# Kernel optimization log

Hardware: AMD Instinct MI355X
Metric: run time of the kernel (lower is better)

The kernel has to match this reference:

```python
import jax, jax.numpy as jnp
import numpy as np

DIM = 2048
DIM_INNER = 4096
D_STATE = 64
D_CONV = 4
HEADDIM = 128
NHEADS = DIM_INNER // HEADDIM  # 32
CHUNK = 256
BATCH = 1
SEQ = 2048
CONV_DIM = DIM_INNER + 2 * D_STATE           # 4224
D_IN_PROJ = 2 * DIM_INNER + 2 * D_STATE + NHEADS  # 8352


def setup_inputs() -> dict:
    key = jax.random.key(0)
    ks = jax.random.split(key, 8)
    x = jax.random.normal(ks[0], (BATCH, SEQ, DIM), jnp.float32)
    in_proj_w = jax.random.normal(ks[1], (D_IN_PROJ, DIM), jnp.float32) * 0.02
    conv_w = jax.random.normal(ks[2], (CONV_DIM, D_CONV), jnp.float32) * 0.2
    conv_b = jnp.zeros((CONV_DIM,), jnp.float32)
    dt_bias = jax.random.normal(ks[3], (NHEADS,), jnp.float32) * 0.1
    A_log = jnp.log(jax.random.uniform(ks[4], (NHEADS,), jnp.float32, 1.0, 16.0))
    D = jnp.ones((NHEADS,), jnp.float32)
    norm_w = jnp.ones((DIM_INNER,), jnp.float32)
    out_proj_w = jax.random.normal(ks[5], (DIM, DIM_INNER), jnp.float32) * 0.02
    return dict(x=x, in_proj_w=in_proj_w, conv_w=conv_w, conv_b=conv_b,
                dt_bias=dt_bias, A_log=A_log, D=D, norm_w=norm_w,
                out_proj_w=out_proj_w)


def _segsum(a):
    # a: [..., T]; out[..., i, j] = sum_{k=j+1..i} a[..., k] for i>=j else -inf
    T = a.shape[-1]
    cs = jnp.cumsum(a, axis=-1)
    seg = cs[..., :, None] - cs[..., None, :]
    mask = jnp.tril(jnp.ones((T, T), bool))
    return jnp.where(mask, seg, -jnp.inf)


def _ssd(x, A, Bm, Cm, chunk):
    # x: [b,l,h,p], A: [b,l,h], Bm/Cm: [b,l,n] (ngroups=1, group dim squeezed)
    b, l, h, p = x.shape
    n = Bm.shape[-1]
    c = l // chunk
    x = x.reshape(b, c, chunk, h, p)
    A = A.reshape(b, c, chunk, h).transpose(0, 3, 1, 2)  # [b,h,c,l]
    Bm = Bm.reshape(b, c, chunk, n)
    Cm = Cm.reshape(b, c, chunk, n)
    A_cumsum = jnp.cumsum(A, axis=-1)                    # [b,h,c,l]
    Lmat = jnp.exp(_segsum(A))                           # [b,h,c,l,l]
    # intra-chunk (diagonal) contribution
    Y_diag = jnp.einsum('bcln,bcsn,bhcls,bcshp->bclhp', Cm, Bm, Lmat, x)
    # per-chunk states
    decay_states = jnp.exp(A_cumsum[..., -1:] - A_cumsum)
    states = jnp.einsum('bcln,bhcl,bclhp->bchpn', Bm, decay_states, x)
    states = jnp.concatenate([jnp.zeros_like(states[:, :1]), states], axis=1)
    # inter-chunk recurrence
    A_last = jnp.pad(A_cumsum[..., -1], ((0, 0), (0, 0), (1, 0)))  # [b,h,c+1]
    decay_chunk = jnp.exp(_segsum(A_last))
    new_states = jnp.einsum('bhzc,bchpn->bzhpn', decay_chunk, states)
    states, final_state = new_states[:, :-1], new_states[:, -1]
    # state -> output (off-diagonal) contribution
    state_decay_out = jnp.exp(A_cumsum)
    Y_off = jnp.einsum('bcln,bchpn,bhcl->bclhp', Cm, states, state_decay_out)
    return (Y_diag + Y_off).reshape(b, l, h, p), final_state


def reference(x, in_proj_w, conv_w, conv_b, dt_bias, A_log, D, norm_w, out_proj_w):
    B, L, _ = x.shape
    zxbcdt = x @ in_proj_w.T                              # [B,L,8352]
    z = zxbcdt[..., :DIM_INNER]
    xBC = zxbcdt[..., DIM_INNER:DIM_INNER + CONV_DIM]
    dt = jax.nn.softplus(zxbcdt[..., -NHEADS:] + dt_bias)  # [B,L,H]
    # causal depthwise conv1d over time (pad d_conv-1 on the left)
    xc = xBC.transpose(0, 2, 1)                           # [B,conv_dim,L]
    xc = jax.lax.conv_general_dilated(
        xc, conv_w[:, None, :], (1,), [(D_CONV - 1, 0)],
        dimension_numbers=('NCH', 'OIH', 'NCH'), feature_group_count=CONV_DIM)
    xc = xc + conv_b[None, :, None]
    xBC = jax.nn.silu(xc).transpose(0, 2, 1)              # [B,L,conv_dim]
    xs = xBC[..., :DIM_INNER].reshape(B, L, NHEADS, HEADDIM)
    Bmat = xBC[..., DIM_INNER:DIM_INNER + D_STATE]
    Cmat = xBC[..., DIM_INNER + D_STATE:]
    A = -jnp.exp(A_log)                                   # [H]
    y, final_state = _ssd(xs * dt[..., None], A * dt, Bmat, Cmat, CHUNK)
    y = y + xs * D[:, None]
    y = y.reshape(B, L, DIM_INNER)
    # gated RMSNorm: x * silu(z), then rms_norm with weight
    g = y * jax.nn.silu(z)
    g = g * jax.lax.rsqrt(jnp.mean(g * g, axis=-1, keepdims=True) + 1e-5) * norm_w
    return g @ out_proj_w.T
```

## Files before the change

kernel.cpp:

```cpp
#include <hip/hip_runtime.h>

typedef short v8s __attribute__((ext_vector_type(8)));
typedef float v4f __attribute__((ext_vector_type(4)));

#define L_SEQ  2048
#define DPROJ  8352
#define CONVD  4224
#define DIN    4096
#define NH     32
#define HD     128
#define NSTATE 64
#define NCHUNK 8
#define CKLEN  256

#define GLOAD_LDS16(gp, lp) \
  __builtin_amdgcn_global_load_lds((const __attribute__((address_space(1))) void*)(gp), \
                                   (__attribute__((address_space(3))) void*)(lp), 16, 0, 0)

__device__ __forceinline__ unsigned short to_bf16(float f) {
  unsigned u = __float_as_uint(f);
  return (unsigned short)((u + 0x7fffu + ((u >> 16) & 1u)) >> 16);
}

__global__ void cvt_bf16_kernel(const float* __restrict__ in,
                                unsigned short* __restrict__ out, int n) {
  int i = (blockIdx.x * 256 + threadIdx.x) * 8;
  if (i + 8 <= n) {
    float4 a = *(const float4*)(in + i);
    float4 b = *(const float4*)(in + i + 4);
    v8s r;
    r[0] = (short)to_bf16(a.x); r[1] = (short)to_bf16(a.y);
    r[2] = (short)to_bf16(a.z); r[3] = (short)to_bf16(a.w);
    r[4] = (short)to_bf16(b.x); r[5] = (short)to_bf16(b.y);
    r[6] = (short)to_bf16(b.z); r[7] = (short)to_bf16(b.w);
    *(v8s*)(out + i) = r;
  }
}


#define BAR    __builtin_amdgcn_s_barrier()
#define SCHEDB __builtin_amdgcn_sched_barrier(0)
#define LGKM0  asm volatile("s_waitcnt lgkmcnt(0)" ::: "memory")
#define VMCNT4 asm volatile("s_waitcnt vmcnt(4)" ::: "memory")

#define RDA(bu, mh) do { \
  _Pragma("unroll") \
  for (int i = 0; i < 4; ++i) \
    _Pragma("unroll") \
    for (int s = 0; s < 2; ++s) { \
      int row_ = (mh) * 128 + wm * 64 + i * 16 + lrow; \
      int off_ = row_ * 128 + s * 64 + lquad * 16; \
      off_ ^= ((off_ >> 7) & 7) << 4; \
      a8[i][s] = *(const v8s*)((const char*)smem + (bu) * 32768 + off_); \
    } \
} while (0)

#define RDB(bu, nh) do { \
  _Pragma("unroll") \
  for (int j = 0; j < 2; ++j) \
    _Pragma("unroll") \
    for (int s = 0; s < 2; ++s) { \
      int row_ = (nh) * 128 + wn * 32 + j * 16 + lrow; \
      int off_ = row_ * 128 + s * 64 + lquad * 16; \
      off_ ^= ((off_ >> 7) & 7) << 4; \
      b8[nh][j][s] = *(const v8s*)((const char*)smem + 65536 + (bu) * 32768 + off_); \
    } \
} while (0)

#define MM(mh, nh) do { \
  __builtin_amdgcn_s_setprio(1); \
  _Pragma("unroll") \
  for (int i = 0; i < 4; ++i) \
    _Pragma("unroll") \
    for (int j = 0; j < 2; ++j) \
      _Pragma("unroll") \
      for (int s = 0; s < 2; ++s) \
        acc[(mh)*4+i][(nh)*2+j] = __builtin_amdgcn_mfma_f32_16x16x32_bf16( \
            a8[i][s], b8[(nh)][j][s], acc[(mh)*4+i][(nh)*2+j], 0, 0, 0); \
  __builtin_amdgcn_s_setprio(0); \
} while (0)

#define KSTEP(BU, BN_, T1, T2) do { \
  RDA(BU, 0); RDB(BU, 0); \
  stA(BN_, 1, T1); \
  BAR; LGKM0; SCHEDB; \
  MM(0, 0); \
  BAR; \
  RDB(BU, 1); \
  stB(BN_, 1, T1); \
  BAR; LGKM0; SCHEDB; \
  MM(0, 1); \
  BAR; \
  RDA(BU, 1); \
  stA(BU, 0, T2); \
  BAR; LGKM0; SCHEDB; \
  MM(1, 0); \
  BAR; \
  stB(BU, 0, T2); \
  BAR; \
  MM(1, 1); \
  SCHEDB; VMCNT4; SCHEDB; \
  BAR; SCHEDB; \
} while (0)

__global__ __launch_bounds__(512, 2) void gemm_nt_256(
    const unsigned short* __restrict__ A, const unsigned short* __restrict__ B,
    float* __restrict__ C, int lda, int ldb, int ldc, int ncols, int K)
{
  __shared__ unsigned short smem[65536];
  const int m0 = blockIdx.x * 256;
  const int n0 = blockIdx.y * 256;
  A += (size_t)blockIdx.z * K;
  B += (size_t)blockIdx.z * K;
  C += (size_t)blockIdx.z * 2048 * (size_t)ldc;
  const int tid = threadIdx.x;
  const int wave = tid >> 6, lane = tid & 63;
  const int wm = wave >> 2, wn = wave & 3;
  const int lrow = lane & 15, lquad = lane >> 4;
  const int NT = K >> 6;

  v4f acc[8][4] = {};
  v8s a8[4][2];
  v8s b8[2][2][2];

  auto stA = [&](int bu, int h, int kt) {
#pragma unroll
    for (int g = 0; g < 2; ++g) {
      int lin = h * 16384 + g * 8192 + tid * 16;
      int sw = lin ^ (((lin >> 7) & 7) << 4);
      int row = sw >> 7;
      const unsigned short* src = A + (size_t)(m0 + row) * lda + kt * 64 + ((sw & 127) >> 1);
      GLOAD_LDS16(src, smem + bu * 16384 + h * 8192 + g * 4096 + wave * 512);
    }
  };
  auto stB = [&](int bu, int h, int kt) {
#pragma unroll
    for (int g = 0; g < 2; ++g) {
      int lin = h * 16384 + g * 8192 + tid * 16;
      int sw = lin ^ (((lin >> 7) & 7) << 4);
      int brow = n0 + (sw >> 7);
      if (brow >= ncols) brow = ncols - 1;
      const unsigned short* src = B + (size_t)brow * ldb + kt * 64 + ((sw & 127) >> 1);
      GLOAD_LDS16(src, smem + 32768 + bu * 16384 + h * 8192 + g * 4096 + wave * 512);
    }
  };

  stA(0, 0, 0); stA(0, 1, 0); stB(0, 0, 0); stB(0, 1, 0);
  stA(1, 0, 1); stB(1, 0, 1);
  SCHEDB; VMCNT4; SCHEDB; BAR; SCHEDB;

#pragma unroll 1
  for (int tt = 0; tt < NT; tt += 2) {
    {
      int t1 = tt + 1;
      int t2 = (tt + 2 < NT) ? tt + 2 : NT - 1;
      KSTEP(0, 1, t1, t2);
    }
    {
      int t1 = (tt + 2 < NT) ? tt + 2 : NT - 1;
      int t2 = (tt + 3 < NT) ? tt + 3 : NT - 1;
      KSTEP(1, 0, t1, t2);
    }
  }

#pragma unroll
  for (int mh = 0; mh < 2; ++mh)
#pragma unroll
    for (int i = 0; i < 4; ++i) {
      int grow = m0 + mh * 128 + wm * 64 + i * 16 + lquad * 4;
#pragma unroll
      for (int nh = 0; nh < 2; ++nh)
#pragma unroll
        for (int j = 0; j < 2; ++j) {
          int gcol = n0 + nh * 128 + wn * 32 + j * 16 + lrow;
          if (gcol < ncols) {
#pragma unroll
            for (int r = 0; r < 4; ++r)
              C[(size_t)(grow + r) * ldc + gcol] = acc[mh * 4 + i][nh * 2 + j][r];
          }
        }
    }
}

__global__ __launch_bounds__(256) void reduce_k4_kernel(
    const float* __restrict__ p, float* __restrict__ out, int n)
{
  const int S = 4194304;
  int i = (blockIdx.x * 256 + threadIdx.x) * 4;
  if (i + 4 <= n) {
    float4 a = *(const float4*)(p + i);
    float4 b = *(const float4*)(p + S + i);
    float4 c = *(const float4*)(p + 2 * S + i);
    float4 d = *(const float4*)(p + 3 * S + i);
    float4 o;
    o.x = a.x + b.x + c.x + d.x;
    o.y = a.y + b.y + c.y + d.y;
    o.z = a.z + b.z + c.z + d.z;
    o.w = a.w + b.w + c.w + d.w;
    *(float4*)(out + i) = o;
  }
}

__global__ __launch_bounds__(256) void gemm_nt_64tail(
    const unsigned short* __restrict__ A, const unsigned short* __restrict__ B,
    float* __restrict__ C, int Ncols, int ldc, int K)
{
  __shared__ unsigned short As[64 * 32];
  __shared__ unsigned short Bs[128 * 32];
  const int m0 = blockIdx.x * 64;
  const int n0 = blockIdx.y * 128;
  const int tid = threadIdx.x;
  const int wave = tid >> 6, lane = tid & 63;
  const int wm = (wave & 1) * 32, wn = (wave >> 1) * 64;
  const int lrow = lane & 15, lquad = lane >> 4;

  v4f acc[2][4] = {};

  for (int k0 = 0; k0 < K; k0 += 32) {
    __syncthreads();
    {
      int e = wave * 64 + lane;
      int row = e >> 2;
      int kq = (e & 3) * 8;
      const unsigned short* ap = A + (size_t)(m0 + row) * K + k0 + kq;
      GLOAD_LDS16(ap, As + wave * 512);
    }
#pragma unroll
    for (int r = 0; r < 2; ++r) {
      int e = wave * 128 + r * 64 + lane;
      int row = e >> 2;
      int kq = (e & 3) * 8;
      int br = n0 + row; if (br >= Ncols) br = Ncols - 1;
      const unsigned short* bp = B + (size_t)br * K + k0 + kq;
      GLOAD_LDS16(bp, Bs + wave * 1024 + r * 512);
    }
    __syncthreads();
    v8s af[2], bfr[4];
#pragma unroll
    for (int i = 0; i < 2; ++i)
      af[i] = *(const v8s*)&As[(wm + i * 16 + lrow) * 32 + lquad * 8];
#pragma unroll
    for (int j = 0; j < 4; ++j)
      bfr[j] = *(const v8s*)&Bs[(wn + j * 16 + lrow) * 32 + lquad * 8];
#pragma unroll
    for (int i = 0; i < 2; ++i)
#pragma unroll
      for (int j = 0; j < 4; ++j)
        acc[i][j] = __builtin_amdgcn_mfma_f32_16x16x32_bf16(af[i], bfr[j], acc[i][j], 0, 0, 0);
  }

#pragma unroll
  for (int i = 0; i < 2; ++i) {
    int grow = m0 + wm + i * 16 + lquad * 4;
#pragma unroll
    for (int j = 0; j < 4; ++j) {
      int gcol = n0 + wn + j * 16 + lrow;
      if (gcol < Ncols) {
#pragma unroll
        for (int r = 0; r < 4; ++r)
          C[(size_t)(grow + r) * ldc + gcol] = acc[i][j][r];
      }
    }
  }
}

__global__ __launch_bounds__(256) void conv_silu_kernel(
    const float* __restrict__ zx, const float* __restrict__ cw,
    const float* __restrict__ cb, float* __restrict__ out)
{
  const int l0 = blockIdx.x * 32, c0 = blockIdx.y * 128;
  const int tid = threadIdx.x;
  __shared__ float zs[35][128];
  __shared__ float cwl[4][128];
  __shared__ float cbl[128];
  for (int e = tid; e < 35 * 128; e += 256) {
    int k = e >> 7, cc = e & 127;
    int l = l0 + k - 3;
    zs[k][cc] = (l >= 0) ? zx[(size_t)l * DPROJ + DIN + c0 + cc] : 0.f;
  }
  for (int e = tid; e < 512; e += 256)
    cwl[e & 3][e >> 2] = cw[c0 * 4 + e];
  if (tid < 128) cbl[tid] = cb[c0 + tid];
  __syncthreads();
#pragma unroll
  for (int i = 0; i < 16; ++i) {
    int idx = i * 256 + tid;
    int ll = idx >> 7, cc = idx & 127;
    float acc = cbl[cc];
#pragma unroll
    for (int j = 0; j < 4; ++j)
      acc += zs[ll + j][cc] * cwl[j][cc];
    out[(size_t)(l0 + ll) * CONVD + c0 + cc] = acc / (1.f + __expf(-acc));
  }
}

__global__ void dt_kernel(const float* __restrict__ zx,
                          const float* __restrict__ dtb,
                          float* __restrict__ dt)
{
  int e = blockIdx.x * 256 + threadIdx.x;
  int l = e >> 5, h = e & 31;
  float v = zx[(size_t)l * DPROJ + (DPROJ - NH) + h] + dtb[h];
  dt[e] = (v > 20.f) ? v : log1pf(__expf(v));
}

__global__ void acum_kernel(const float* __restrict__ dt,
                            const float* __restrict__ alog,
                            float* __restrict__ acum)
{
  int h = blockIdx.x & 31, c = blockIdx.x >> 5;
  int t = threadIdx.x;
  int l = c * CKLEN + t;
  float A = -__expf(alog[h]);
  __shared__ float s[256];
  s[t] = A * dt[l * NH + h];
  __syncthreads();
  for (int off = 1; off < 256; off <<= 1) {
    float add = (t >= off) ? s[t - off] : 0.f;
    __syncthreads();
    s[t] += add;
    __syncthreads();
  }
  acum[h * L_SEQ + l] = s[t];
}

__global__ __launch_bounds__(256) void prep_kernel(
    const float* __restrict__ xbc, const float* __restrict__ dt,
    const float* __restrict__ acum, unsigned short* __restrict__ Xd,
    unsigned short* __restrict__ Btw, unsigned short* __restrict__ Cbf)
{
  const int h = blockIdx.x & 31, c = blockIdx.x >> 5;
  const int tid = threadIdx.x;
  __shared__ float Ac[256], Dt[256], Wd[256];
  __shared__ float Xs[32][129];
  __shared__ float Bs2[32][65];
  int l = c * CKLEN + tid;
  float a = acum[h * L_SEQ + l];
  Ac[tid] = a;
  Dt[tid] = dt[l * NH + h];
  __syncthreads();
  float alast = Ac[255];
  Wd[tid] = __expf(fminf(alast - a, 0.f));
  __syncthreads();
  unsigned short* XdB = Xd + (size_t)(c * NH + h) * (HD * CKLEN);
  unsigned short* BtB = Btw + (size_t)(c * NH + h) * (NSTATE * CKLEN);
  for (int t0 = 0; t0 < CKLEN; t0 += 32) {
    for (int e = tid; e < 32 * 128; e += 256) {
      int tt = e >> 7, pp = e & 127;
      Xs[tt][pp] = xbc[(size_t)(c * CKLEN + t0 + tt) * CONVD + h * HD + pp];
    }
    for (int e = tid; e < 32 * 64; e += 256) {
      int tt = e >> 6, nn = e & 63;
      Bs2[tt][nn] = xbc[(size_t)(c * CKLEN + t0 + tt) * CONVD + DIN + nn];
    }
    __syncthreads();
    {
      int p = tid >> 1, th = (tid & 1) * 16;
      v8s r0, r1;
#pragma unroll
      for (int k = 0; k < 8; ++k) {
        r0[k] = (short)to_bf16(Xs[th + k][p] * Dt[t0 + th + k]);
        r1[k] = (short)to_bf16(Xs[th + 8 + k][p] * Dt[t0 + th + 8 + k]);
      }
      *(v8s*)&XdB[p * CKLEN + t0 + th] = r0;
      *(v8s*)&XdB[p * CKLEN + t0 + th + 8] = r1;
    }
    {
      int n = tid >> 2, tq = (tid & 3) * 8;
      v8s r;
#pragma unroll
      for (int k = 0; k < 8; ++k)
        r[k] = (short)to_bf16(Bs2[tq + k][n] * Wd[t0 + tq + k]);
      *(v8s*)&BtB[n * CKLEN + t0 + tq] = r;
    }
    __syncthreads();
  }
  if (h == 0) {
    for (int e = tid; e < CKLEN * NSTATE; e += 256) {
      int ll = e >> 6, nn = e & 63;
      Cbf[(size_t)c * (CKLEN * NSTATE) + e] =
          to_bf16(xbc[(size_t)(c * CKLEN + ll) * CONVD + DIN + NSTATE + nn]);
    }
  }
}

__global__ __launch_bounds__(256) void g_kernel(const float* __restrict__ xbc,
                                                float* __restrict__ G)
{
  int c = blockIdx.z;
  int l0 = blockIdx.y * 64, s0 = blockIdx.x * 64;
  __shared__ float Cs[64][65];
  __shared__ float Bs[64][65];
  int tid = threadIdx.x;
  for (int e = tid; e < 64 * 64; e += 256) {
    int r = e >> 6, k = e & 63;
    Cs[r][k] = xbc[(size_t)(c * CKLEN + l0 + r) * CONVD + DIN + NSTATE + k];
    Bs[r][k] = xbc[(size_t)(c * CKLEN + s0 + r) * CONVD + DIN + k];
  }
  __syncthreads();
  int tx = tid & 15, ty = tid >> 4;
  float acc[4][4] = {};
  for (int k = 0; k < 64; ++k) {
    float a[4], b[4];
#pragma unroll
    for (int i = 0; i < 4; ++i) a[i] = Cs[ty * 4 + i][k];
#pragma unroll
    for (int j = 0; j < 4; ++j) b[j] = Bs[tx * 4 + j][k];
#pragma unroll
    for (int i = 0; i < 4; ++i)
#pragma unroll
      for (int j = 0; j < 4; ++j) acc[i][j] += a[i] * b[j];
  }
  for (int i = 0; i < 4; ++i)
    for (int j = 0; j < 4; ++j)
      G[((size_t)c * CKLEN + l0 + ty * 4 + i) * CKLEN + s0 + tx * 4 + j] = acc[i][j];
}

__global__ __launch_bounds__(256) void gexp_kernel_v2(
    const float* __restrict__ G, const float* __restrict__ acum,
    unsigned short* __restrict__ Gexp)
{
  const int b = blockIdx.x;
  const int si = b & 7, li = (b >> 3) & 3, c = b >> 5;
  const int l0 = li * 64, s0 = si * 32;
  const int tid = threadIdx.x;
  const int r = tid >> 2, sc = (tid & 3) * 8;

  if (s0 >= l0 + 64) {
    v8s z = {};
    for (int h = 0; h < NH; ++h)
      *(v8s*)&Gexp[(size_t)(c * NH + h) * 65536 + (size_t)(l0 + r) * 256 + s0 + sc] = z;
    return;
  }

  __shared__ float Gs[64 * 32];
  __shared__ float Acl[32][64];
  __shared__ float Acs[32][32];
  for (int e = tid; e < 2048; e += 256) {
    int rr = e >> 5, cc = e & 31;
    Gs[e] = G[(size_t)c * 65536 + (size_t)(l0 + rr) * 256 + s0 + cc];
  }
  for (int e = tid; e < 2048; e += 256) {
    int hh = e >> 6, rr = e & 63;
    Acl[hh][rr] = acum[hh * L_SEQ + c * CKLEN + l0 + rr];
  }
  for (int e = tid; e < 1024; e += 256) {
    int hh = e >> 5, ss = e & 31;
    Acs[hh][ss] = acum[hh * L_SEQ + c * CKLEN + s0 + ss];
  }
  __syncthreads();

  float g8[8];
#pragma unroll
  for (int k = 0; k < 8; ++k) g8[k] = Gs[r * 32 + sc + k];

  for (int h = 0; h < NH; ++h) {
    float al = Acl[h][r];
    v8s o;
#pragma unroll
    for (int k = 0; k < 8; ++k) {
      int s = s0 + sc + k;
      float m = 0.f;
      if (s <= l0 + r) m = g8[k] * __expf(fminf(al - Acs[h][sc + k], 0.f));
      o[k] = (short)to_bf16(m);
    }
    *(v8s*)&Gexp[(size_t)(c * NH + h) * 65536 + (size_t)(l0 + r) * 256 + s0 + sc] = o;
  }
}

__global__ __launch_bounds__(256) void states_kernel_v2(
    const unsigned short* __restrict__ Xd, const unsigned short* __restrict__ Btw,
    float* __restrict__ st)
{
  const int h = blockIdx.x & 31, c = blockIdx.x >> 5;
  const int tid = threadIdx.x;
  const int wave = tid >> 6, lane = tid & 63;
  const int wm = (wave & 1) * 64, wn = (wave >> 1) * 32;
  const int lrow = lane & 15, lquad = lane >> 4;

  __shared__ unsigned short As[128 * 32];
  __shared__ unsigned short Bs[64 * 32];
  const unsigned short* Ab = Xd + (size_t)(c * NH + h) * (HD * CKLEN);
  const unsigned short* Bb = Btw + (size_t)(c * NH + h) * (NSTATE * CKLEN);

  v4f acc[4][2] = {};

  for (int k0 = 0; k0 < CKLEN; k0 += 32) {
    __syncthreads();
#pragma unroll
    for (int r = 0; r < 2; ++r) {
      int e = wave * 128 + r * 64 + lane;
      int row = e >> 2, kq = (e & 3) * 8;
      GLOAD_LDS16(Ab + (size_t)row * CKLEN + k0 + kq, As + wave * 1024 + r * 512);
    }
    {
      int e = wave * 64 + lane;
      int row = e >> 2, kq = (e & 3) * 8;
      GLOAD_LDS16(Bb + (size_t)row * CKLEN + k0 + kq, Bs + wave * 512);
    }
    __syncthreads();
    v8s af[4], bfr[2];
#pragma unroll
    for (int i = 0; i < 4; ++i)
      af[i] = *(const v8s*)&As[(wm + i * 16 + lrow) * 32 + lquad * 8];
#pragma unroll
    for (int j = 0; j < 2; ++j)
      bfr[j] = *(const v8s*)&Bs[(wn + j * 16 + lrow) * 32 + lquad * 8];
#pragma unroll
    for (int i = 0; i < 4; ++i)
#pragma unroll
      for (int j = 0; j < 2; ++j)
        acc[i][j] = __builtin_amdgcn_mfma_f32_16x16x32_bf16(af[i], bfr[j], acc[i][j], 0, 0, 0);
  }

  float* outp = st + (size_t)(c * NH + h) * (HD * NSTATE);
#pragma unroll
  for (int i = 0; i < 4; ++i) {
    int p0 = wm + i * 16 + lquad * 4;
#pragma unroll
    for (int j = 0; j < 2; ++j) {
      int n = wn + j * 16 + lrow;
#pragma unroll
      for (int r = 0; r < 4; ++r)
        outp[(size_t)(p0 + r) * NSTATE + n] = acc[i][j][r];
    }
  }
}

__global__ void scan_kernel(const float* __restrict__ acum,
                            const float* __restrict__ st,
                            unsigned short* __restrict__ spbf)
{
  int e = blockIdx.x * 256 + threadIdx.x;
  int h = e >> 13;
  float running = 0.f;
#pragma unroll
  for (int c = 0; c < NCHUNK; ++c) {
    spbf[(size_t)c * 262144 + e] = to_bf16(running);
    float dec = __expf(fminf(acum[h * L_SEQ + c * CKLEN + 255], 0.f));
    running = running * dec + st[(size_t)c * 262144 + e];
  }
}

__global__ __launch_bounds__(256) void y_kernel_v2(
    const unsigned short* __restrict__ Gexp, const unsigned short* __restrict__ Xd,
    const unsigned short* __restrict__ Cbf, const unsigned short* __restrict__ spbf,
    const float* __restrict__ xbc, const float* __restrict__ acum,
    const float* __restrict__ Dp, float* __restrict__ Y)
{
  const int b = blockIdx.x, h = blockIdx.y, c = blockIdx.z;
  const int tid = threadIdx.x;
  const int wave = tid >> 6, lane = tid & 63;
  const int wm = wave * 32;
  const int lrow = lane & 15, lquad = lane >> 4;

  __shared__ unsigned short As[128 * 32];
  __shared__ unsigned short Bs[128 * 32];

  v4f acc[2][8] = {};

  const unsigned short* Ca = Cbf + (size_t)c * (CKLEN * NSTATE) + (size_t)b * 128 * NSTATE;
  const unsigned short* Sb = spbf + (size_t)(c * NH + h) * (HD * NSTATE);
  for (int n0 = 0; n0 < NSTATE; n0 += 32) {
    __syncthreads();
#pragma unroll
    for (int r = 0; r < 2; ++r) {
      int e = wave * 128 + r * 64 + lane;
      int row = e >> 2, kq = (e & 3) * 8;
      GLOAD_LDS16(Ca + (size_t)row * NSTATE + n0 + kq, As + wave * 1024 + r * 512);
      GLOAD_LDS16(Sb + (size_t)row * NSTATE + n0 + kq, Bs + wave * 1024 + r * 512);
    }
    __syncthreads();
    v8s af[2], bfr[8];
#pragma unroll
    for (int i = 0; i < 2; ++i)
      af[i] = *(const v8s*)&As[(wm + i * 16 + lrow) * 32 + lquad * 8];
#pragma unroll
    for (int j = 0; j < 8; ++j)
      bfr[j] = *(const v8s*)&Bs[(j * 16 + lrow) * 32 + lquad * 8];
#pragma unroll
    for (int i = 0; i < 2; ++i)
#pragma unroll
      for (int j = 0; j < 8; ++j)
        acc[i][j] = __builtin_amdgcn_mfma_f32_16x16x32_bf16(af[i], bfr[j], acc[i][j], 0, 0, 0);
  }

#pragma unroll
  for (int i = 0; i < 2; ++i) {
#pragma unroll
    for (int r = 0; r < 4; ++r) {
      int Lg = c * CKLEN + b * 128 + wm + i * 16 + lquad * 4 + r;
      float eA = __expf(fminf(acum[h * L_SEQ + Lg], 0.f));
#pragma unroll
      for (int j = 0; j < 8; ++j) acc[i][j][r] *= eA;
    }
  }

  const unsigned short* Ga = Gexp + (size_t)(c * NH + h) * (CKLEN * CKLEN)
                           + (size_t)b * 128 * CKLEN;
  const unsigned short* Xb = Xd + (size_t)(c * NH + h) * (HD * CKLEN);

  const int smax = (b + 1) * 128;
  for (int s0 = 0; s0 < smax; s0 += 32) {
    __syncthreads();
#pragma unroll
    for (int r = 0; r < 2; ++r) {
      int e = wave * 128 + r * 64 + lane;
      int row = e >> 2, kq = (e & 3) * 8;
      GLOAD_LDS16(Ga + (size_t)row * CKLEN + s0 + kq, As + wave * 1024 + r * 512);
      GLOAD_LDS16(Xb + (size_t)row * CKLEN + s0 + kq, Bs + wave * 1024 + r * 512);
    }
    __syncthreads();
    if (s0 <= b * 128 + wm + 31) {
      v8s af[2], bfr[8];
#pragma unroll
      for (int i = 0; i < 2; ++i)
        af[i] = *(const v8s*)&As[(wm + i * 16 + lrow) * 32 + lquad * 8];
#pragma unroll
      for (int j = 0; j < 8; ++j)
        bfr[j] = *(const v8s*)&Bs[(j * 16 + lrow) * 32 + lquad * 8];
#pragma unroll
      for (int i = 0; i < 2; ++i)
#pragma unroll
        for (int j = 0; j < 8; ++j)
          acc[i][j] = __builtin_amdgcn_mfma_f32_16x16x32_bf16(af[i], bfr[j], acc[i][j], 0, 0, 0);
    }
  }

  const float Dh = Dp[h];
#pragma unroll
  for (int i = 0; i < 2; ++i) {
#pragma unroll
    for (int j = 0; j < 8; ++j) {
      int p = j * 16 + lrow;
#pragma unroll
      for (int r = 0; r < 4; ++r) {
        int Lg = c * CKLEN + b * 128 + wm + i * 16 + lquad * 4 + r;
        float xs = xbc[(size_t)Lg * CONVD + h * HD + p];
        Y[(size_t)Lg * DIN + h * HD + p] = acc[i][j][r] + Dh * xs;
      }
    }
  }
}

__global__ __launch_bounds__(256) void norm_gate_kernel(const float* __restrict__ Y,
                                                        const float* __restrict__ zx,
                                                        const float* __restrict__ nw,
                                                        unsigned short* __restrict__ gbf)
{
  int l = blockIdx.x;
  int t = threadIdx.x;
  float g[16];
  float ss = 0.f;
#pragma unroll
  for (int i = 0; i < 16; ++i) {
    int idx = i * 256 + t;
    float z = zx[(size_t)l * DPROJ + idx];
    float y = Y[(size_t)l * DIN + idx];
    float gv = y * (z / (1.f + __expf(-z)));
    g[i] = gv;
    ss += gv * gv;
  }
#pragma unroll
  for (int off = 32; off > 0; off >>= 1) ss += __shfl_down(ss, off);
  __shared__ float red[4];
  if ((t & 63) == 0) red[t >> 6] = ss;
  __syncthreads();
  float total = red[0] + red[1] + red[2] + red[3];
  float scale = rsqrtf(total / (float)DIN + 1e-5f);
#pragma unroll
  for (int i = 0; i < 16; ++i) {
    int idx = i * 256 + t;
    gbf[(size_t)l * DIN + idx] = to_bf16(g[i] * scale * nw[idx]);
  }
}

extern "C" void kernel_launch(void* const* d_in, const int* in_sizes, int n_in,
                              void* d_out, int out_size, void* d_ws, size_t ws_size,
                              hipStream_t stream) {
  const float* x    = (const float*)d_in[0];
  const float* w1   = (const float*)d_in[1];
  const float* cw   = (const float*)d_in[2];
  const float* cb   = (const float*)d_in[3];
  const float* dtb  = (const float*)d_in[4];
  const float* alog = (const float*)d_in[5];
  const float* Dp   = (const float*)d_in[6];
  const float* nw   = (const float*)d_in[7];
  const float* w2   = (const float*)d_in[8];
  float* out = (float*)d_out;
  float* ws  = (float*)d_ws;

  unsigned short* xbf  = (unsigned short*)(ws + 0);
  unsigned short* w1bf = (unsigned short*)(ws + 2097152);
  unsigned short* Gexp = (unsigned short*)(ws + 0);
  unsigned short* Btw  = (unsigned short*)(ws + 8388608);
  unsigned short* w2bf = (unsigned short*)(ws + 10649600);
  float* zx   = ws + 14843904;
  float* part = ws + 14843904;
  float* xbc  = ws + 31948800;
  float* dt   = ws + 40599552;
  float* acum = ws + 40665088;
  float* G    = ws + 40730624;
  float* st   = ws + 41254912;
  float* Y    = ws + 43352064;
  unsigned short* gbf  = (unsigned short*)(ws + 51740672);
  unsigned short* Xd   = (unsigned short*)(ws + 53837824);
  unsigned short* Cbf  = (unsigned short*)(ws + 58032128);
  unsigned short* spbf = (unsigned short*)(ws + 58097664);

  cvt_bf16_kernel<<<4194304 / 2048, 256, 0, stream>>>(x, xbf, 4194304);
  cvt_bf16_kernel<<<17104896 / 2048, 256, 0, stream>>>(w1, w1bf, 17104896);
  cvt_bf16_kernel<<<8388608 / 2048, 256, 0, stream>>>(w2, w2bf, 8388608);

  gemm_nt_256<<<dim3(8, 32, 1), 512, 0, stream>>>(
      xbf, w1bf, zx, 2048, 2048, 8352, 8352, 2048);
  gemm_nt_64tail<<<dim3(32, 2), 256, 0, stream>>>(
      xbf, w1bf + (size_t)8192 * 2048, zx + 8192, 160, 8352, 2048);

  conv_silu_kernel<<<dim3(64, 33), 256, 0, stream>>>(zx, cw, cb, xbc);
  dt_kernel<<<(L_SEQ * NH) / 256, 256, 0, stream>>>(zx, dtb, dt);
  acum_kernel<<<NCHUNK * NH, 256, 0, stream>>>(dt, alog, acum);

  prep_kernel<<<NCHUNK * NH, 256, 0, stream>>>(xbc, dt, acum, Xd, Btw, Cbf);
  g_kernel<<<dim3(4, 4, NCHUNK), 256, 0, stream>>>(xbc, G);
  gexp_kernel_v2<<<256, 256, 0, stream>>>(G, acum, Gexp);

  states_kernel_v2<<<NCHUNK * NH, 256, 0, stream>>>(Xd, Btw, st);
  scan_kernel<<<262144 / 256, 256, 0, stream>>>(acum, st, spbf);
  y_kernel_v2<<<dim3(2, NH, NCHUNK), 256, 0, stream>>>(Gexp, Xd, Cbf, spbf, xbc, acum, Dp, Y);

  norm_gate_kernel<<<L_SEQ, 256, 0, stream>>>(Y, zx, nw, gbf);

  gemm_nt_256<<<dim3(8, 8, 4), 512, 0, stream>>>(
      gbf, w2bf, part, 4096, 4096, 2048, 2048, 1024);
  reduce_k4_kernel<<<4194304 / 1024, 256, 0, stream>>>(part, out, 4194304);
}
```

Measured before the change: 454.5 us.

## Split-K the in_proj tail GEMM and swizzle 256-tile GEMM workgroup order

The 160-column tail of the input projection now runs as a 4-way split-K GEMM (256 blocks instead of 64). Partial sums go into the scratch state buffer and a new reduce kernel adds them and writes the result into zx. Separately, the 256x256 GEMM remaps its block indices with an 8-way interleave so that blocks running at the same time share A/B tiles in cache. The cost is an extra kernel launch and a partial-sum round trip through memory, and the swizzle assumes the 2D grid count divides by 8.

```diff
diff --git a/kernel.cpp b/kernel.cpp
--- a/kernel.cpp
+++ b/kernel.cpp
@@ -108,8 +108,13 @@
     float* __restrict__ C, int lda, int ldb, int ldc, int ncols, int K)
 {
   __shared__ unsigned short smem[65536];
-  const int m0 = blockIdx.x * 256;
-  const int n0 = blockIdx.y * 256;
+  const int nwgx = gridDim.x;
+  const int nwg  = nwgx * gridDim.y;
+  const int lin  = blockIdx.x + nwgx * blockIdx.y;
+  const int q    = nwg >> 3;
+  const int swz  = (lin & 7) * q + (lin >> 3);
+  const int m0 = (swz % nwgx) * 256;
+  const int n0 = (swz / nwgx) * 256;
   A += (size_t)blockIdx.z * K;
   B += (size_t)blockIdx.z * K;
   C += (size_t)blockIdx.z * 2048 * (size_t)ldc;
@@ -126,8 +131,8 @@
   auto stA = [&](int bu, int h, int kt) {
 #pragma unroll
     for (int g = 0; g < 2; ++g) {
-      int lin = h * 16384 + g * 8192 + tid * 16;
-      int sw = lin ^ (((lin >> 7) & 7) << 4);
+      int lin2 = h * 16384 + g * 8192 + tid * 16;
+      int sw = lin2 ^ (((lin2 >> 7) & 7) << 4);
       int row = sw >> 7;
       const unsigned short* src = A + (size_t)(m0 + row) * lda + kt * 64 + ((sw & 127) >> 1);
       GLOAD_LDS16(src, smem + bu * 16384 + h * 8192 + g * 4096 + wave * 512);
@@ -136,8 +141,8 @@
   auto stB = [&](int bu, int h, int kt) {
 #pragma unroll
     for (int g = 0; g < 2; ++g) {
-      int lin = h * 16384 + g * 8192 + tid * 16;
-      int sw = lin ^ (((lin >> 7) & 7) << 4);
+      int lin2 = h * 16384 + g * 8192 + tid * 16;
+      int sw = lin2 ^ (((lin2 >> 7) & 7) << 4);
       int brow = n0 + (sw >> 7);
       if (brow >= ncols) brow = ncols - 1;
       const unsigned short* src = B + (size_t)brow * ldb + kt * 64 + ((sw & 127) >> 1);
@@ -201,14 +206,37 @@
   }
 }
 
+__global__ __launch_bounds__(256) void reduce_tail_kernel(
+    const float* __restrict__ p, float* __restrict__ zxt)
+{
+  const int S = 2048 * 160;
+  int i = (blockIdx.x * 256 + threadIdx.x) * 4;
+  if (i + 4 <= S) {
+    float4 a = *(const float4*)(p + i);
+    float4 b = *(const float4*)(p + S + i);
+    float4 c = *(const float4*)(p + 2 * S + i);
+    float4 d = *(const float4*)(p + 3 * S + i);
+    float4 o;
+    o.x = a.x + b.x + c.x + d.x;
+    o.y = a.y + b.y + c.y + d.y;
+    o.z = a.z + b.z + c.z + d.z;
+    o.w = a.w + b.w + c.w + d.w;
+    int row = i / 160, col = i % 160;
+    *(float4*)(zxt + (size_t)row * DPROJ + col) = o;
+  }
+}
+
 __global__ __launch_bounds__(256) void gemm_nt_64tail(
     const unsigned short* __restrict__ A, const unsigned short* __restrict__ B,
-    float* __restrict__ C, int Ncols, int ldc, int K)
+    float* __restrict__ C, int Ncols, int ldcp, int lda, int Kslice)
 {
   __shared__ unsigned short As[64 * 32];
   __shared__ unsigned short Bs[128 * 32];
   const int m0 = blockIdx.x * 64;
   const int n0 = blockIdx.y * 128;
+  A += (size_t)blockIdx.z * Kslice;
+  B += (size_t)blockIdx.z * Kslice;
+  C += (size_t)blockIdx.z * 2048 * (size_t)ldcp;
   const int tid = threadIdx.x;
   const int wave = tid >> 6, lane = tid & 63;
   const int wm = (wave & 1) * 32, wn = (wave >> 1) * 64;
@@ -216,13 +244,13 @@
 
   v4f acc[2][4] = {};
 
-  for (int k0 = 0; k0 < K; k0 += 32) {
+  for (int k0 = 0; k0 < Kslice; k0 += 32) {
     __syncthreads();
     {
       int e = wave * 64 + lane;
       int row = e >> 2;
       int kq = (e & 3) * 8;
-      const unsigned short* ap = A + (size_t)(m0 + row) * K + k0 + kq;
+      const unsigned short* ap = A + (size_t)(m0 + row) * lda + k0 + kq;
       GLOAD_LDS16(ap, As + wave * 512);
     }
 #pragma unroll
@@ -231,7 +259,7 @@
       int row = e >> 2;
       int kq = (e & 3) * 8;
       int br = n0 + row; if (br >= Ncols) br = Ncols - 1;
-      const unsigned short* bp = B + (size_t)br * K + k0 + kq;
+      const unsigned short* bp = B + (size_t)br * lda + k0 + kq;
       GLOAD_LDS16(bp, Bs + wave * 1024 + r * 512);
     }
     __syncthreads();
@@ -258,7 +286,7 @@
       if (gcol < Ncols) {
 #pragma unroll
         for (int r = 0; r < 4; ++r)
-          C[(size_t)(grow + r) * ldc + gcol] = acc[i][j][r];
+          C[(size_t)(grow + r) * ldcp + gcol] = acc[i][j][r];
       }
     }
   }
@@ -714,8 +742,9 @@
 
   gemm_nt_256<<<dim3(8, 32, 1), 512, 0, stream>>>(
       xbf, w1bf, zx, 2048, 2048, 8352, 8352, 2048);
-  gemm_nt_64tail<<<dim3(32, 2), 256, 0, stream>>>(
-      xbf, w1bf + (size_t)8192 * 2048, zx + 8192, 160, 8352, 2048);
+  gemm_nt_64tail<<<dim3(32, 2, 4), 256, 0, stream>>>(
+      xbf, w1bf + (size_t)8192 * 2048, st, 160, 160, 2048, 512);
+  reduce_tail_kernel<<<320, 256, 0, stream>>>(st, zx + 8192);
 
   conv_silu_kernel<<<dim3(64, 33), 256, 0, stream>>>(zx, cw, cb, xbc);
   dt_kernel<<<(L_SEQ * NH) / 256, 256, 0, stream>>>(zx, dtb, dt);
```

Result: faster. 426.3 us (-6.2%).
